# Performance work log

Measured on AMD Instinct MI355X. Metric: run time of the kernel, lower is better.

## Reference

```python
import jax, jax.numpy as jnp
import numpy as np

B, H, T, IN, OUT = 128, 512, 1024, 8, 2


def _likelihood(tm, arms):
    # tm: (B,), arms: (B,2) -> squared normalized timing mismatch, zeroed where tm==0
    pr = jnp.square((tm[:, None] - arms) / (0.15 * arms))
    return jnp.where(tm[:, None] == 0, jnp.zeros_like(pr), pr)


def setup_inputs() -> dict:
    key = jax.random.key(0)
    k_in, k_wi, k_wr, k_wk = jax.random.split(key, 4)
    # arms/timing strictly positive in [0.5, 1.5) to avoid division blow-up
    inputs = jax.random.uniform(k_in, (B, IN, T), dtype=jnp.float32) + 0.5
    W_in = jax.random.normal(k_wi, (H, IN), dtype=jnp.float32) / np.sqrt(IN)
    b_in = jnp.zeros((H,), jnp.float32)
    W_rec = jax.random.normal(k_wr, (H, H), dtype=jnp.float32) / np.sqrt(H)
    b_rec = jnp.zeros((H,), jnp.float32)
    W_key = jax.random.normal(k_wk, (OUT, H), dtype=jnp.float32) / np.sqrt(H)
    b_key = jnp.zeros((OUT,), jnp.float32)
    return {"inputs": inputs, "W_in": W_in, "b_in": b_in, "W_rec": W_rec,
            "b_rec": b_rec, "W_key": W_key, "b_key": b_key}


def reference(inputs, W_in, b_in, W_rec, b_rec, W_key, b_key):
    Bs, _, Ts = inputs.shape
    Hs = W_rec.shape[0]
    xs = jnp.transpose(inputs[:, :, 1:], (2, 0, 1))  # (T-1, B, 8), loop starts at t=1
    h0 = jnp.zeros((Bs, Hs), inputs.dtype)
    key0 = jnp.ones((Bs,), inputs.dtype)  # key_h_pre initialized to ones

    def step(carry, x):
        h_pre, key_pre = carry
        arms_pri = x[:, :2]
        arms_sec = x[:, 2:6]
        tm = x[:, 6:8]
        # gate secondary arms by previous key value
        arms_sum = arms_sec[:, :2] * key_pre[:, None] + arms_sec[:, 2:] * (1.0 - key_pre[:, None])
        pr = jnp.concatenate([_likelihood(tm[:, 0], arms_pri),
                              _likelihood(tm[:, 1], arms_sum)], axis=1)  # (B,4)
        h = jnp.tanh(x @ W_in.T + b_in + h_pre @ W_rec.T + b_rec)  # (B,H)
        key = jax.nn.sigmoid(h @ W_key.T + b_key)  # (B,2)
        return (h, key[:, 0]), (key, pr, h)

    _, (keys_s, prs_s, hs_s) = jax.lax.scan(step, (h0, key0), xs)

    def to_out(y):
        # (T-1, B, C) -> (B, C, T) with zeros at t=0 (buffers were torch.zeros)
        y = jnp.transpose(y, (1, 2, 0))
        return jnp.concatenate([jnp.zeros(y.shape[:2] + (1,), y.dtype), y], axis=2)

    keys = to_out(keys_s)   # (B, 2, T)
    prs = to_out(prs_s)     # (B, 4, T)
    hs = to_out(hs_s)       # (B, H, T)
    return keys, prs, hs
```

## Files before the change

kernel.cpp:

```cpp
#include <hip/hip_runtime.h>
#include <math.h>


#define BB  128
#define HH  512
#define TT  1024
#define SS  1023
#define NIN 8
#define NG  32
#define BPG 4
#define NJB 8
#define JBS 64
#define NTH 512
#define HBH (NG * BPG * HH)

#define BAR_LGKM() do {                                          \
    __builtin_amdgcn_sched_barrier(0);                           \
    __asm__ volatile("s_waitcnt lgkmcnt(0)" ::: "memory");       \
    __builtin_amdgcn_s_barrier();                                \
    __builtin_amdgcn_sched_barrier(0);                           \
} while (0)

__launch_bounds__(NTH, 2)
__global__ void rnn_persist(const float* __restrict__ inputs,
                            const float* __restrict__ W_in,
                            const float* __restrict__ b_in,
                            const float* __restrict__ W_rec,
                            const float* __restrict__ b_rec,
                            const float* __restrict__ W_key,
                            const float* __restrict__ b_key,
                            float* __restrict__ out,
                            float* __restrict__ hbuf)
{
    const int tid  = threadIdx.x;
    const int lane = tid & 63;
    const int wv   = tid >> 6;
    const int g    = blockIdx.x & (NG - 1);
    const int jb   = blockIdx.x >> 5;
    const int b0   = g * BPG;
    const int j0   = jb * JBS;

    float* keys_out = out;
    float* prs_out  = out + (size_t)BB * 2 * TT;
    float* hs_out   = out + (size_t)BB * 6 * TT;

    __shared__ float lds_chunk[NJB][BPG][JBS];
    __shared__ float lds_part[8][BPG][JBS];
    __shared__ float lds_hs[BPG * JBS * 33];
    __shared__ float lds_win[NIN][JBS];
    __shared__ float lds_wkey[2 * HH];
    __shared__ float lds_bias[JBS];
    __shared__ float lds_x2[2][BPG][NIN];
    __shared__ float lds_key[BPG];
    __shared__ float lds_bkey[2];

    float4 w4[16];
    {
        const float4* wr = (const float4*)(W_rec + (size_t)(j0 + lane) * HH + wv * 64);
        #pragma unroll
        for (int i = 0; i < 16; ++i) w4[i] = wr[i];
    }
    if (tid < NIN * JBS) {
        int i = tid >> 6, j = tid & 63;
        lds_win[i][j] = W_in[(size_t)(j0 + j) * NIN + i];
    }
    for (int i = tid; i < 2 * HH; i += NTH) lds_wkey[i] = W_key[i];
    if (tid < JBS) lds_bias[tid] = b_in[j0 + tid] + b_rec[j0 + tid];
    if (tid < BPG) lds_key[tid] = 1.0f;
    if (tid < 2)   lds_bkey[tid] = b_key[tid];
    for (int r = tid; r < BPG * JBS; r += NTH) lds_hs[r * 33] = 0.0f;

    if (jb == 0) {
        if (tid < BPG * 2) keys_out[((size_t)(b0 + (tid >> 1)) * 2 + (tid & 1)) * TT] = 0.0f;
        if (tid < BPG * 4) prs_out [((size_t)(b0 + (tid >> 2)) * 4 + (tid & 3)) * TT] = 0.0f;
    }

    const float* psrc = hbuf + (size_t)g * (BPG * HH) + wv * JBS + lane;
    float*       pdst = hbuf + (size_t)g * (BPG * HH);

    __syncthreads();

    for (int s = 0; s < SS; ++s) {
        if (tid >= NTH - 32) {
            int t = tid - (NTH - 32), b = t >> 3, i = t & 7;
            lds_x2[s & 1][b][i] = inputs[(size_t)(b0 + b) * NIN * TT + (size_t)i * TT + (s + 1)];
        }
        if (s > 0) {
            const float* p = psrc + (size_t)((s - 1) & 1) * HBH;
            const int neg = ((s - 1) >> 1) & 1;
            const float off = neg ? -3.0f : 3.0f;
            float v0, v1, v2, v3;
            int rdy;
            do {
                v0 = __hip_atomic_load(p,          __ATOMIC_RELAXED, __HIP_MEMORY_SCOPE_AGENT);
                v1 = __hip_atomic_load(p + HH,     __ATOMIC_RELAXED, __HIP_MEMORY_SCOPE_AGENT);
                v2 = __hip_atomic_load(p + 2 * HH, __ATOMIC_RELAXED, __HIP_MEMORY_SCOPE_AGENT);
                v3 = __hip_atomic_load(p + 3 * HH, __ATOMIC_RELAXED, __HIP_MEMORY_SCOPE_AGENT);
                if (neg)
                    rdy = (v0 <= -1.5f) & (v1 <= -1.5f) & (v2 <= -1.5f) & (v3 <= -1.5f);
                else
                    rdy = (v0 >=  1.5f) & (v1 >=  1.5f) & (v2 >=  1.5f) & (v3 >=  1.5f);
            } while (!__all(rdy));
            lds_chunk[wv][0][lane] = v0 - off;
            lds_chunk[wv][1][lane] = v1 - off;
            lds_chunk[wv][2][lane] = v2 - off;
            lds_chunk[wv][3][lane] = v3 - off;
        } else {
            lds_chunk[wv][0][lane] = 0.0f;
            lds_chunk[wv][1][lane] = 0.0f;
            lds_chunk[wv][2][lane] = 0.0f;
            lds_chunk[wv][3][lane] = 0.0f;
        }

        {
            const float4* hp = (const float4*)&lds_chunk[wv][0][0];
            float a0 = 0.f, a1 = 0.f, a2 = 0.f, a3 = 0.f;
            #pragma unroll
            for (int kk = 0; kk < 16; ++kk) {
                float4 w  = w4[kk];
                float4 x0 = hp[kk], x1 = hp[16 + kk], x2 = hp[32 + kk], x3 = hp[48 + kk];
                a0 += w.x * x0.x + w.y * x0.y + w.z * x0.z + w.w * x0.w;
                a1 += w.x * x1.x + w.y * x1.y + w.z * x1.z + w.w * x1.w;
                a2 += w.x * x2.x + w.y * x2.y + w.z * x2.z + w.w * x2.w;
                a3 += w.x * x3.x + w.y * x3.y + w.z * x3.z + w.w * x3.w;
            }
            lds_part[wv][0][lane] = a0;
            lds_part[wv][1][lane] = a1;
            lds_part[wv][2][lane] = a2;
            lds_part[wv][3][lane] = a3;
        }
        BAR_LGKM();

        if (tid < BPG * JBS) {
            int b = tid >> 6, j = tid & 63;
            float pre = lds_bias[j];
            #pragma unroll
            for (int w = 0; w < 8; ++w) pre += lds_part[w][b][j];
            #pragma unroll
            for (int i = 0; i < NIN; ++i) pre += lds_x2[s & 1][b][i] * lds_win[i][j];
            float hv = tanhf(pre);
            float enc = hv + (((s >> 1) & 1) ? -3.0f : 3.0f);
            __hip_atomic_store(&pdst[(size_t)(s & 1) * HBH + (size_t)b * HH + j0 + j], enc,
                               __ATOMIC_RELAXED, __HIP_MEMORY_SCOPE_AGENT);
            lds_hs[(b * JBS + j) * 33 + ((s + 1) & 31)] = hv;
        } else if (jb == 0 && s > 0) {
            int t2  = tid - 256;
            int dot = t2 >> 5;
            int b = dot >> 1, c = dot & 1, seg = t2 & 31;
            float p = 0.f;
            #pragma unroll
            for (int m = 0; m < 16; ++m) {
                int k = seg + 32 * m;
                p += lds_chunk[k >> 6][b][k & 63] * lds_wkey[c * HH + k];
            }
            #pragma unroll
            for (int off = 16; off > 0; off >>= 1) p += __shfl_down(p, off, 32);
            if (seg == 0) {
                float kv = 1.0f / (1.0f + __expf(-(p + lds_bkey[c])));
                keys_out[((size_t)(b0 + b) * 2 + c) * TT + s] = kv;
                if (c == 0) lds_key[b] = kv;
            }
        }
        BAR_LGKM();

        if (jb == 0 && tid < BPG * 4) {
            int b = tid >> 2, c = tid & 3;
            float kv = lds_key[b];
            const float* xb = lds_x2[s & 1][b];
            float tmv, arm;
            if (c < 2) { tmv = xb[6]; arm = xb[c]; }
            else       { tmv = xb[7]; arm = xb[c] * kv + xb[c + 2] * (1.0f - kv); }
            float r = (tmv - arm) / (0.15f * arm);
            prs_out[((size_t)(b0 + b) * 4 + c) * TT + (s + 1)] = (tmv == 0.0f) ? 0.0f : r * r;
        }

        if (((s + 1) & 31) == 31) {
            int u0 = s - 30;
            int r = tid >> 1, half = tid & 1;
            int b = r >> 6, j = r & 63;
            float* dst = hs_out + ((size_t)(b0 + b) * HH + j0 + j) * TT + u0 + half * 16;
            const float* src = &lds_hs[r * 33 + half * 16];
            #pragma unroll
            for (int q = 0; q < 4; ++q) {
                float4 v = { src[4 * q], src[4 * q + 1], src[4 * q + 2], src[4 * q + 3] };
                *(float4*)(dst + 4 * q) = v;
            }
        }
    }

    if (jb == 0 && tid >= 256) {
        int t2  = tid - 256;
        int dot = t2 >> 5;
        int b = dot >> 1, c = dot & 1, seg = t2 & 31;
        const float* hb = hbuf + (size_t)((SS - 1) & 1) * HBH
                        + (size_t)g * (BPG * HH) + (size_t)b * HH;
        float p = 0.f;
        #pragma unroll
        for (int m = 0; m < 16; ++m) {
            int k = seg + 32 * m;
            float v;
            do {
                v = __hip_atomic_load(hb + k, __ATOMIC_RELAXED, __HIP_MEMORY_SCOPE_AGENT);
            } while (!(v <= -1.5f));
            p += (v + 3.0f) * lds_wkey[c * HH + k];
        }
        #pragma unroll
        for (int off = 16; off > 0; off >>= 1) p += __shfl_down(p, off, 32);
        if (seg == 0) {
            float kv = 1.0f / (1.0f + __expf(-(p + lds_bkey[c])));
            keys_out[((size_t)(b0 + b) * 2 + c) * TT + (TT - 1)] = kv;
        }
    }
}

extern "C" void kernel_launch(void* const* d_in, const int* in_sizes, int n_in,
                              void* d_out, int out_size, void* d_ws, size_t ws_size,
                              hipStream_t stream) {
    const float* inputs = (const float*)d_in[0];
    const float* W_in   = (const float*)d_in[1];
    const float* b_in   = (const float*)d_in[2];
    const float* W_rec  = (const float*)d_in[3];
    const float* b_rec  = (const float*)d_in[4];
    const float* W_key  = (const float*)d_in[5];
    const float* b_key  = (const float*)d_in[6];
    float* outp = (float*)d_out;

    float* hbuf = (float*)d_ws;
    hipMemsetAsync(d_ws, 0, (size_t)2 * HBH * sizeof(float), stream);

    rnn_persist<<<dim3(NG * NJB), dim3(NTH), 0, stream>>>(
        inputs, W_in, b_in, W_rec, b_rec, W_key, b_key, outp, hbuf);
}
```

Before: 2.664 ms.

## Repartition RNN blocks to 2 batches x 128 units and broadcast h via readlane

```diff
diff --git a/kernel.cpp b/kernel.cpp
--- a/kernel.cpp
+++ b/kernel.cpp
@@ -7,10 +7,10 @@
 #define TT  1024
 #define SS  1023
 #define NIN 8
-#define NG  32
-#define BPG 4
-#define NJB 8
-#define JBS 64
+#define NG  64
+#define BPG 2
+#define NJB 4
+#define JBS 128
 #define NTH 512
 #define HBH (NG * BPG * HH)
 
@@ -20,6 +20,10 @@
     __builtin_amdgcn_s_barrier();                                \
     __builtin_amdgcn_sched_barrier(0);                           \
 } while (0)
+
+__device__ __forceinline__ float bcast(float v, int ln) {
+    return __int_as_float(__builtin_amdgcn_readlane(__float_as_int(v), ln));
+}
 
 __launch_bounds__(NTH, 2)
 __global__ void rnn_persist(const float* __restrict__ inputs,
@@ -36,7 +40,7 @@
     const int lane = tid & 63;
     const int wv   = tid >> 6;
     const int g    = blockIdx.x & (NG - 1);
-    const int jb   = blockIdx.x >> 5;
+    const int jb   = blockIdx.x >> 6;
     const int b0   = g * BPG;
     const int j0   = jb * JBS;
 
@@ -44,7 +48,7 @@
     float* prs_out  = out + (size_t)BB * 2 * TT;
     float* hs_out   = out + (size_t)BB * 6 * TT;
 
-    __shared__ float lds_chunk[NJB][BPG][JBS];
+    __shared__ float lds_chunk[8][BPG][64];
     __shared__ float lds_part[8][BPG][JBS];
     __shared__ float lds_hs[BPG * JBS * 33];
     __shared__ float lds_win[NIN][JBS];
@@ -54,14 +58,15 @@
     __shared__ float lds_key[BPG];
     __shared__ float lds_bkey[2];
 
-    float4 w4[16];
+    float4 w0[16], w1[16];
     {
-        const float4* wr = (const float4*)(W_rec + (size_t)(j0 + lane) * HH + wv * 64);
+        const float4* wr0 = (const float4*)(W_rec + (size_t)(j0 + lane) * HH + wv * 64);
+        const float4* wr1 = (const float4*)(W_rec + (size_t)(j0 + 64 + lane) * HH + wv * 64);
         #pragma unroll
-        for (int i = 0; i < 16; ++i) w4[i] = wr[i];
-    }
-    if (tid < NIN * JBS) {
-        int i = tid >> 6, j = tid & 63;
+        for (int i = 0; i < 16; ++i) { w0[i] = wr0[i]; w1[i] = wr1[i]; }
+    }
+    for (int r = tid; r < NIN * JBS; r += NTH) {
+        int i = r & 7, j = r >> 3;
         lds_win[i][j] = W_in[(size_t)(j0 + j) * NIN + i];
     }
     for (int i = tid; i < 2 * HH; i += NTH) lds_wkey[i] = W_key[i];
@@ -75,64 +80,66 @@
         if (tid < BPG * 4) prs_out [((size_t)(b0 + (tid >> 2)) * 4 + (tid & 3)) * TT] = 0.0f;
     }
 
-    const float* psrc = hbuf + (size_t)g * (BPG * HH) + wv * JBS + lane;
+    const float* psrc = hbuf + (size_t)g * (BPG * HH) + wv * 64 + lane;
     float*       pdst = hbuf + (size_t)g * (BPG * HH);
 
     __syncthreads();
 
     for (int s = 0; s < SS; ++s) {
-        if (tid >= NTH - 32) {
-            int t = tid - (NTH - 32), b = t >> 3, i = t & 7;
+        if (tid >= NTH - 16) {
+            int t = tid - (NTH - 16), b = t >> 3, i = t & 7;
             lds_x2[s & 1][b][i] = inputs[(size_t)(b0 + b) * NIN * TT + (size_t)i * TT + (s + 1)];
         }
+        float h0, h1;
         if (s > 0) {
             const float* p = psrc + (size_t)((s - 1) & 1) * HBH;
             const int neg = ((s - 1) >> 1) & 1;
             const float off = neg ? -3.0f : 3.0f;
-            float v0, v1, v2, v3;
+            float v0, v1;
             int rdy;
             do {
-                v0 = __hip_atomic_load(p,          __ATOMIC_RELAXED, __HIP_MEMORY_SCOPE_AGENT);
-                v1 = __hip_atomic_load(p + HH,     __ATOMIC_RELAXED, __HIP_MEMORY_SCOPE_AGENT);
-                v2 = __hip_atomic_load(p + 2 * HH, __ATOMIC_RELAXED, __HIP_MEMORY_SCOPE_AGENT);
-                v3 = __hip_atomic_load(p + 3 * HH, __ATOMIC_RELAXED, __HIP_MEMORY_SCOPE_AGENT);
-                if (neg)
-                    rdy = (v0 <= -1.5f) & (v1 <= -1.5f) & (v2 <= -1.5f) & (v3 <= -1.5f);
-                else
-                    rdy = (v0 >=  1.5f) & (v1 >=  1.5f) & (v2 >=  1.5f) & (v3 >=  1.5f);
+                v0 = __hip_atomic_load(p,      __ATOMIC_RELAXED, __HIP_MEMORY_SCOPE_AGENT);
+                v1 = __hip_atomic_load(p + HH, __ATOMIC_RELAXED, __HIP_MEMORY_SCOPE_AGENT);
+                rdy = neg ? ((v0 <= -1.5f) & (v1 <= -1.5f))
+                          : ((v0 >=  1.5f) & (v1 >=  1.5f));
             } while (!__all(rdy));
-            lds_chunk[wv][0][lane] = v0 - off;
-            lds_chunk[wv][1][lane] = v1 - off;
-            lds_chunk[wv][2][lane] = v2 - off;
-            lds_chunk[wv][3][lane] = v3 - off;
+            h0 = v0 - off;
+            h1 = v1 - off;
         } else {
-            lds_chunk[wv][0][lane] = 0.0f;
-            lds_chunk[wv][1][lane] = 0.0f;
-            lds_chunk[wv][2][lane] = 0.0f;
-            lds_chunk[wv][3][lane] = 0.0f;
+            h0 = 0.0f;
+            h1 = 0.0f;
+        }
+        if (jb == 0) {
+            lds_chunk[wv][0][lane] = h0;
+            lds_chunk[wv][1][lane] = h1;
         }
 
         {
-            const float4* hp = (const float4*)&lds_chunk[wv][0][0];
-            float a0 = 0.f, a1 = 0.f, a2 = 0.f, a3 = 0.f;
-            #pragma unroll
-            for (int kk = 0; kk < 16; ++kk) {
-                float4 w  = w4[kk];
-                float4 x0 = hp[kk], x1 = hp[16 + kk], x2 = hp[32 + kk], x3 = hp[48 + kk];
-                a0 += w.x * x0.x + w.y * x0.y + w.z * x0.z + w.w * x0.w;
-                a1 += w.x * x1.x + w.y * x1.y + w.z * x1.z + w.w * x1.w;
-                a2 += w.x * x2.x + w.y * x2.y + w.z * x2.z + w.w * x2.w;
-                a3 += w.x * x3.x + w.y * x3.y + w.z * x3.z + w.w * x3.w;
-            }
-            lds_part[wv][0][lane] = a0;
-            lds_part[wv][1][lane] = a1;
-            lds_part[wv][2][lane] = a2;
-            lds_part[wv][3][lane] = a3;
+            float a00 = 0.f, a01 = 0.f, a10 = 0.f, a11 = 0.f;
+            #pragma unroll
+            for (int q = 0; q < 16; ++q) {
+                const float* wa = (const float*)&w0[q];
+                const float* wb = (const float*)&w1[q];
+                #pragma unroll
+                for (int c = 0; c < 4; ++c) {
+                    const int ln = q * 4 + c;
+                    float s0 = bcast(h0, ln);
+                    float s1 = bcast(h1, ln);
+                    float wva = wa[c];
+                    float wvb = wb[c];
+                    a00 += wva * s0; a01 += wva * s1;
+                    a10 += wvb * s0; a11 += wvb * s1;
+                }
+            }
+            lds_part[wv][0][lane]      = a00;
+            lds_part[wv][1][lane]      = a01;
+            lds_part[wv][0][lane + 64] = a10;
+            lds_part[wv][1][lane + 64] = a11;
         }
         BAR_LGKM();
 
         if (tid < BPG * JBS) {
-            int b = tid >> 6, j = tid & 63;
+            int b = tid >> 7, j = tid & 127;
             float pre = lds_bias[j];
             #pragma unroll
             for (int w = 0; w < 8; ++w) pre += lds_part[w][b][j];
@@ -143,7 +150,7 @@
             __hip_atomic_store(&pdst[(size_t)(s & 1) * HBH + (size_t)b * HH + j0 + j], enc,
                                __ATOMIC_RELAXED, __HIP_MEMORY_SCOPE_AGENT);
             lds_hs[(b * JBS + j) * 33 + ((s + 1) & 31)] = hv;
-        } else if (jb == 0 && s > 0) {
+        } else if (jb == 0 && s > 0 && tid < 384) {
             int t2  = tid - 256;
             int dot = t2 >> 5;
             int b = dot >> 1, c = dot & 1, seg = t2 & 31;
@@ -177,7 +184,7 @@
         if (((s + 1) & 31) == 31) {
             int u0 = s - 30;
             int r = tid >> 1, half = tid & 1;
-            int b = r >> 6, j = r & 63;
+            int b = r >> 7, j = r & 127;
             float* dst = hs_out + ((size_t)(b0 + b) * HH + j0 + j) * TT + u0 + half * 16;
             const float* src = &lds_hs[r * 33 + half * 16];
             #pragma unroll
@@ -188,7 +195,7 @@
         }
     }
 
-    if (jb == 0 && tid >= 256) {
+    if (jb == 0 && tid >= 256 && tid < 384) {
         int t2  = tid - 256;
         int dot = t2 >> 5;
         int b = dot >> 1, c = dot & 1, seg = t2 & 31;
```

Measured after the change: 2.571 ms. 1.04x faster.
